# Kernel optimization log

Hardware: AMD Instinct MI355X
Metric: run time of the kernel (lower is better)

The kernel has to match this reference:

```python
import jax, jax.numpy as jnp
import numpy as np

N_HEAD = 8
N_EMBD = 768
T_MAX = 1024


def setup_inputs() -> dict:
    key = jax.random.key(0)
    ks = jax.random.split(key, 5)
    B, T, C = 8, 1024, N_EMBD
    x = jax.random.normal(ks[0], (B, T, C), dtype=jnp.float32)
    c_attn_weight = jax.random.normal(ks[1], (3 * C, C), dtype=jnp.float32) * (1.0 / np.sqrt(C))
    c_attn_bias = jax.random.normal(ks[2], (3 * C,), dtype=jnp.float32) * 0.02
    c_proj_weight = jax.random.normal(ks[3], (C, C), dtype=jnp.float32) * (1.0 / np.sqrt(C))
    c_proj_bias = jax.random.normal(ks[4], (C,), dtype=jnp.float32) * 0.02
    bias = jnp.tril(jnp.ones((T_MAX, T_MAX), dtype=jnp.int32))[None, None]  # (1,1,Tmax,Tmax)
    return {
        "x": x,
        "c_attn_weight": c_attn_weight,
        "c_attn_bias": c_attn_bias,
        "c_proj_weight": c_proj_weight,
        "c_proj_bias": c_proj_bias,
        "bias": bias,
    }


def reference(x, c_attn_weight, c_attn_bias, c_proj_weight, c_proj_bias, bias):
    B, T, C = x.shape
    H = N_HEAD
    D = C // H  # head dim
    qkv = jnp.einsum("btc,fc->btf", x, c_attn_weight) + c_attn_bias  # (B,T,3C)
    q, k, v = jnp.split(qkv, 3, axis=-1)
    q = q.reshape(B, T, H, D).transpose(0, 2, 1, 3)  # (B,H,T,D)
    k = k.reshape(B, T, H, D).transpose(0, 2, 1, 3)
    v = v.reshape(B, T, H, D).transpose(0, 2, 1, 3)
    att = jnp.einsum("bhqd,bhkd->bhqk", q, k) * (1.0 / np.sqrt(D))  # (B,H,T,T)
    mask = bias[:, :, :T, :T] == 0
    att = jnp.where(mask, jnp.float32(-jnp.inf), att)
    att = jax.nn.softmax(att, axis=-1)
    y = jnp.einsum("bhqk,bhkd->bhqd", att, v)  # (B,H,T,D)
    y = y.transpose(0, 2, 1, 3).reshape(B, T, C)
    y = jnp.einsum("btc,fc->btf", y, c_proj_weight) + c_proj_bias
    return y
```

## Files before the change

### kernel.cpp

```cpp
#include <hip/hip_runtime.h>
#include <hip/hip_bf16.h>
#include <stdint.h>


typedef unsigned short ushort_t;
typedef __attribute__((ext_vector_type(8))) short short8;
typedef __attribute__((ext_vector_type(4))) float floatx4;
typedef __attribute__((ext_vector_type(4))) unsigned short ushort4v;

#define MFMA16(a, b, c) __builtin_amdgcn_mfma_f32_16x16x32_bf16(a, b, c, 0, 0, 0)
#define NEG_BIG (-1e30f)

__device__ __forceinline__ unsigned short f2bf(float f) {
  union { float f; unsigned int u; } v; v.f = f;
  unsigned int r = (v.u + 0x7FFFu + ((v.u >> 16) & 1u)) >> 16;
  return (unsigned short)r;
}

__device__ __forceinline__ unsigned int packbf2(float a, float b) {
  union { __hip_bfloat162 h; unsigned int u; } cv;
  cv.h = __float22bfloat162_rn(make_float2(a, b));
  return cv.u;
}

#define GLOAD16(src, dst)                                              \
  __builtin_amdgcn_global_load_lds(                                    \
      (const __attribute__((address_space(1))) void*)(src),            \
      (__attribute__((address_space(3))) void*)(dst), 16, 0, 0)

#define WAITBAR_LGKM(VM)                                               \
  do {                                                                 \
    asm volatile("s_waitcnt vmcnt(" #VM ") lgkmcnt(0)" ::: "memory");  \
    __builtin_amdgcn_s_barrier();                                      \
  } while (0)

__global__ __launch_bounds__(256) void cvt3(
    const float* __restrict__ x, const float* __restrict__ wa,
    const float* __restrict__ wp, ushort_t* __restrict__ xb,
    ushort_t* __restrict__ wab, ushort_t* __restrict__ wpb)
{
  const int n1 = (8192 * 768) / 4, n2 = (2304 * 768) / 4;
  int i = blockIdx.x * 256 + threadIdx.x;
  const float* in; ushort_t* out;
  if (i < n1)            { in = x;  out = xb; }
  else if (i < n1 + n2)  { in = wa; out = wab; i -= n1; }
  else                   { in = wp; out = wpb; i -= (n1 + n2); }
  float4 v = *(const float4*)(in + (size_t)i * 4);
  ushort4v o;
  o.x = f2bf(v.x); o.y = f2bf(v.y); o.z = f2bf(v.z); o.w = f2bf(v.w);
  *(ushort4v*)(out + (size_t)i * 4) = o;
}

#define GSTAGE(LA, LB, OFF)                                            \
  do {                                                                 \
    GLOAD16(gA + (OFF), &LA[wid * 512]);                               \
    GLOAD16(gA + (OFF) + (size_t)64 * 768, &LA[wid * 512 + 64 * 32]);  \
    GLOAD16(gB + (OFF), &LB[wid * 512]);                               \
    GLOAD16(gB + (OFF) + (size_t)64 * 768, &LB[wid * 512 + 64 * 32]);  \
  } while (0)

#define GSTEP(LA, LB, OFF, STG, VM)                                    \
  do {                                                                 \
    asm volatile("s_waitcnt vmcnt(" #VM ")" ::: "memory");             \
    __builtin_amdgcn_s_barrier();                                      \
    short8 af[4], bf[4];                                               \
    _Pragma("unroll")                                                  \
    for (int t_ = 0; t_ < 4; ++t_) {                                   \
      af[t_] = *(const short8*)&LA[(wm + t_ * 16 + l15) * 32 + sw];    \
      bf[t_] = *(const short8*)&LB[(wn + t_ * 16 + l15) * 32 + sw];    \
    }                                                                  \
    asm volatile("s_waitcnt lgkmcnt(0)" ::: "memory");                 \
    __builtin_amdgcn_s_barrier();                                      \
    if (STG) GSTAGE(LA, LB, OFF);                                      \
    __builtin_amdgcn_s_setprio(1);                                     \
    _Pragma("unroll")                                                  \
    for (int tm = 0; tm < 4; ++tm)                                     \
      _Pragma("unroll")                                                \
      for (int tn = 0; tn < 4; ++tn)                                   \
        acc[tm][tn] = MFMA16(af[tm], bf[tn], acc[tm][tn]);             \
    __builtin_amdgcn_s_setprio(0);                                     \
  } while (0)

#define GK2(T)                                                         \
  GSTEP(As0, Bs0, ((T) + 2) * 32, 1, 4);                               \
  GSTEP(As1, Bs1, ((T) + 3) * 32, 1, 4);

#define GEMM_KLOOP                                                     \
  GSTAGE(As0, Bs0, 0); GSTAGE(As1, Bs1, 32);                           \
  GK2(0) GK2(2) GK2(4) GK2(6) GK2(8) GK2(10)                           \
  GK2(12) GK2(14) GK2(16) GK2(18) GK2(20)                              \
  GSTEP(As0, Bs0, 0, 0, 4);                                            \
  GSTEP(As1, Bs1, 0, 0, 0);

#define GEMM_DECLS                                                     \
  __shared__ ushort_t As0[128 * 32], As1[128 * 32];                    \
  __shared__ ushort_t Bs0[128 * 32], Bs1[128 * 32];                    \
  const int tid  = threadIdx.x;                                        \
  const int lane = tid & 63;                                           \
  const int l15  = lane & 15;                                          \
  const int quad = lane >> 4;                                          \
  const int wid  = tid >> 6;                                           \
  const int m0 = blockIdx.x * 128;                                     \
  const int n0 = blockIdx.y * 128;                                     \
  const int wm = (wid >> 1) * 64;                                      \
  const int wn = (wid & 1) * 64;                                       \
  const int srow = tid >> 2;                                           \
  const int scol = (((tid & 3) ^ ((srow ^ (srow >> 2)) & 3))) * 8;     \
  const int sw = (quad ^ ((l15 ^ (l15 >> 2)) & 3)) * 8;                \
  floatx4 acc[4][4] = {};

__global__ __launch_bounds__(256) void gemm_qkv(
    const ushort_t* __restrict__ A,
    const ushort_t* __restrict__ W,
    const float* __restrict__ bias,
    ushort_t* __restrict__ QK,
    ushort_t* __restrict__ VT)
{
  GEMM_DECLS;

  const ushort_t* gA = A + (size_t)(m0 + srow) * 768 + scol;
  const ushort_t* gB = W + (size_t)(n0 + srow) * 768 + scol;

  GEMM_KLOOP;

  const float QSCALE = 0.10206207261596577f * 1.4426950408889634f;

#pragma unroll
  for (int tn = 0; tn < 4; ++tn) {
    const int gc = n0 + wn + tn * 16 + l15;
    const float bv = bias[gc];
    const bool isv = (gc >= 1536);
    const bool isq = (gc < 768);
    const int hh = (gc - 1536) / 96, dd = (gc - 1536) % 96;
#pragma unroll
    for (int tm = 0; tm < 4; ++tm) {
      const int gr = m0 + wm + tm * 16 + quad * 4;
      if (!isv) {
#pragma unroll
        for (int r = 0; r < 4; ++r) {
          float val = acc[tm][tn][r] + bv;
          if (isq) val *= QSCALE;
          QK[(size_t)(gr + r) * 1536 + gc] = f2bf(val);
        }
      } else {
        const int bb = gr >> 10, tt = gr & 1023;
        const int tt2 = (tt & ~0x1C) | (((tt >> 4) & 1) << 2) |
                        (((tt >> 2) & 3) << 3);
        ushort4v o;
        o.x = f2bf(acc[tm][tn][0] + bv);
        o.y = f2bf(acc[tm][tn][1] + bv);
        o.z = f2bf(acc[tm][tn][2] + bv);
        o.w = f2bf(acc[tm][tn][3] + bv);
        *(ushort4v*)(VT + (((size_t)(bb * 8 + hh)) * 96 + dd) * 1024 + tt2) = o;
      }
    }
  }
}

__global__ __launch_bounds__(256) void gemm_proj(
    const ushort_t* __restrict__ A,
    const ushort_t* __restrict__ W,
    const float* __restrict__ bias,
    float* __restrict__ C,
    int M, int N)
{
  GEMM_DECLS;

  const ushort_t* gA = A + (size_t)(m0 + srow) * 768 + scol;
  const ushort_t* gB = W + (size_t)(n0 + srow) * 768 + scol;

  GEMM_KLOOP;

#pragma unroll
  for (int tn = 0; tn < 4; ++tn) {
    const int gc = n0 + wn + tn * 16 + l15;
    const float bv = bias[gc];
#pragma unroll
    for (int tm = 0; tm < 4; ++tm) {
      const int gr = m0 + wm + tm * 16 + quad * 4;
#pragma unroll
      for (int r = 0; r < 4; ++r)
        C[(size_t)(gr + r) * N + gc] = acc[tm][tn][r] + bv;
    }
  }
}

#define ATTN_COMPUTE(KS, VTC, K0)                                      \
  do {                                                                 \
    floatx4 s[4] = {};                                                 \
    __builtin_amdgcn_s_setprio(1);                                     \
    _Pragma("unroll")                                                  \
    for (int t = 0; t < 4; ++t) {                                      \
      _Pragma("unroll")                                                \
      for (int c = 0; c < 3; ++c) {                                    \
        short8 kf = *(const short8*)                                   \
            &KS[(t * 16 + l15) * 96 + c * 32 + quad * 8];              \
        s[t] = MFMA16(kf, qf[c], s[t]);                                \
      }                                                                \
    }                                                                  \
    __builtin_amdgcn_s_setprio(0);                                     \
    float p[4][4];                                                     \
    if ((K0) + 64 <= q0w) {                                            \
      _Pragma("unroll")                                                \
      for (int t = 0; t < 4; ++t)                                      \
        _Pragma("unroll")                                              \
        for (int j = 0; j < 4; ++j) p[t][j] = s[t][j];                 \
    } else {                                                           \
      const int kq = (K0) + quad * 4;                                  \
      _Pragma("unroll")                                                \
      for (int t = 0; t < 4; ++t)                                      \
        _Pragma("unroll")                                              \
        for (int j = 0; j < 4; ++j)                                    \
          p[t][j] = (kq + t * 16 + j <= rq) ? s[t][j] : NEG_BIG;       \
    }                                                                  \
    float m0v = fmaxf(fmaxf(p[0][0], p[0][1]), fmaxf(p[0][2], p[0][3]));\
    float m1v = fmaxf(fmaxf(p[1][0], p[1][1]), fmaxf(p[1][2], p[1][3]));\
    float m2v = fmaxf(fmaxf(p[2][0], p[2][1]), fmaxf(p[2][2], p[2][3]));\
    float m3v = fmaxf(fmaxf(p[3][0], p[3][1]), fmaxf(p[3][2], p[3][3]));\
    float mt = fmaxf(fmaxf(m0v, m1v), fmaxf(m2v, m3v));                \
    mt = fmaxf(mt, __shfl_xor(mt, 16));                                \
    mt = fmaxf(mt, __shfl_xor(mt, 32));                                \
    if (!__all(mt - m_i <= 8.0f)) {                                    \
      const float mn = fmaxf(m_i, mt);                                 \
      const float al = __builtin_amdgcn_exp2f(m_i - mn);               \
      m_i = mn;                                                        \
      l_i *= al;                                                       \
      _Pragma("unroll")                                                \
      for (int j = 0; j < 4; ++j) {                                    \
        const float alr = __shfl(al, quad * 4 + j);                    \
        _Pragma("unroll")                                              \
        for (int f = 0; f < 6; ++f) O[f][j] *= alr;                    \
      }                                                                \
    }                                                                  \
    float rs = 0.f;                                                    \
    _Pragma("unroll")                                                  \
    for (int t = 0; t < 4; ++t)                                        \
      _Pragma("unroll")                                                \
      for (int j = 0; j < 4; ++j) {                                    \
        p[t][j] = __builtin_amdgcn_exp2f(p[t][j] - m_i);               \
        rs += p[t][j];                                                 \
      }                                                                \
    rs += __shfl_xor(rs, 16);                                          \
    rs += __shfl_xor(rs, 32);                                          \
    l_i += rs;                                                         \
    union { short8 s8; unsigned int u[4]; } pf0, pf1;                  \
    pf0.u[0] = packbf2(p[0][0], p[0][1]);                              \
    pf0.u[1] = packbf2(p[0][2], p[0][3]);                              \
    pf0.u[2] = packbf2(p[1][0], p[1][1]);                              \
    pf0.u[3] = packbf2(p[1][2], p[1][3]);                              \
    pf1.u[0] = packbf2(p[2][0], p[2][1]);                              \
    pf1.u[1] = packbf2(p[2][2], p[2][3]);                              \
    pf1.u[2] = packbf2(p[3][0], p[3][1]);                              \
    pf1.u[3] = packbf2(p[3][2], p[3][3]);                              \
    __builtin_amdgcn_s_setprio(1);                                     \
    _Pragma("unroll")                                                  \
    for (int f = 0; f < 6; ++f) {                                      \
      short8 vf0 = *(const short8*)&VTC[(f * 16 + l15) * 72 + quad * 8];\
      O[f] = MFMA16(pf0.s8, vf0, O[f]);                                \
      short8 vf1 = *(const short8*)                                    \
          &VTC[(f * 16 + l15) * 72 + 32 + quad * 8];                   \
      O[f] = MFMA16(pf1.s8, vf1, O[f]);                                \
    }                                                                  \
    __builtin_amdgcn_s_setprio(0);                                     \
  } while (0)

#define AITER(KS, VTC, KSN, VTN, K0)                                   \
  do {                                                                 \
    const int k0_ = (K0);                                              \
    const int nk_ = k0_ + 64;                                          \
    WAITBAR_LGKM(3);                                                   \
    _Pragma("unroll")                                                  \
    for (int i = 0; i < 3; ++i) {                                      \
      const int e = ke0 + i * 512;                                     \
      const int kr = e / 96, kc = e % 96;                              \
      GLOAD16(QK + (rowbase + nk_ + kr) * 1536 + 768 + qoff + kc,      \
              &KSN[wid * 1536 + i * 512]);                             \
    }                                                                  \
    ATTN_COMPUTE(KS, VTC, k0_);                                        \
    _Pragma("unroll")                                                  \
    for (int g = 0; g < 3; ++g)                                        \
      *(short8*)&VTN[(g * 32 + vd) * 72 + vkc] = vreg[g];              \
    if (nk_ + 64 < kend) {                                             \
      _Pragma("unroll")                                                \
      for (int g = 0; g < 3; ++g)                                      \
        vreg[g] = *(const short8*)                                     \
            (vtb + (size_t)(g * 32 + vd) * 1024 + nk_ + 64 + vkc);     \
    }                                                                  \
  } while (0)

#define AITER_LAST(KS, VTC, K0)                                        \
  do {                                                                 \
    WAITBAR_LGKM(0);                                                   \
    ATTN_COMPUTE(KS, VTC, (K0));                                       \
  } while (0)

__global__ __launch_bounds__(256) void attn_fused(
    const ushort_t* __restrict__ QK,
    const ushort_t* __restrict__ VT,
    ushort_t* __restrict__ y)
{
  __shared__ ushort_t Ks0[64 * 96], Ks1[64 * 96];
  __shared__ ushort_t Vt0[96 * 72], Vt1[96 * 72];

  const int tid  = threadIdx.x;
  const int lane = tid & 63;
  const int l15  = lane & 15;
  const int quad = lane >> 4;
  const int wid  = tid >> 6;

  const int lin = blockIdx.x + (blockIdx.y << 4);
  const int swz = ((lin & 7) << 7) + (lin >> 3);
  const int chunk = 15 - (swz & 15);
  const int bh = swz >> 4;
  const int b = bh >> 3;
  const int h = bh & 7;
  const int qoff = h * 96;

  const int q0w = chunk * 64 + wid * 16;
  const int kend = chunk * 64 + 64;
  const int rq = q0w + l15;

  const size_t rowbase = (size_t)b * 1024;
  const ushort_t* vtb = VT + (size_t)bh * 96 * 1024;

  const int ke0 = wid * 1536 + lane * 8;
  const int vd  = (tid >> 3);
  const int vkc = (tid & 7) * 8;

  short8 qf[3];
#pragma unroll
  for (int c = 0; c < 3; ++c)
    qf[c] = *(const short8*)(QK + (rowbase + q0w + l15) * 1536 + qoff +
                             c * 32 + quad * 8);

  float m_i = NEG_BIG;
  float l_i = 0.f;
  floatx4 O[6] = {};

  short8 vreg[3];

#pragma unroll
  for (int g = 0; g < 3; ++g)
    vreg[g] = *(const short8*)(vtb + (size_t)(g * 32 + vd) * 1024 + vkc);
#pragma unroll
  for (int i = 0; i < 3; ++i) {
    const int e = ke0 + i * 512;
    const int kr = e / 96, kc = e % 96;
    GLOAD16(QK + (rowbase + kr) * 1536 + 768 + qoff + kc,
            &Ks0[wid * 1536 + i * 512]);
  }
#pragma unroll
  for (int g = 0; g < 3; ++g)
    *(short8*)&Vt0[(g * 32 + vd) * 72 + vkc] = vreg[g];
#pragma unroll
  for (int g = 0; g < 3; ++g)
    vreg[g] = *(const short8*)(vtb + (size_t)(g * 32 + vd) * 1024 + 64 + vkc);

  int k0 = 0;
  while (k0 + 128 < kend) {
    AITER(Ks0, Vt0, Ks1, Vt1, k0);
    AITER(Ks1, Vt1, Ks0, Vt0, k0 + 64);
    k0 += 128;
  }
  if (k0 + 64 < kend) {
    AITER(Ks0, Vt0, Ks1, Vt1, k0);
    AITER_LAST(Ks1, Vt1, k0 + 64);
  } else {
    AITER_LAST(Ks0, Vt0, k0);
  }

  float inv[4];
#pragma unroll
  for (int j = 0; j < 4; ++j) {
    const float lj = __shfl(l_i, quad * 4 + j);
    inv[j] = 1.0f / fmaxf(lj, 1e-20f);
  }
#pragma unroll
  for (int j = 0; j < 4; ++j) {
    const size_t row = rowbase + q0w + quad * 4 + j;
#pragma unroll
    for (int f = 0; f < 6; ++f)
      y[row * 768 + qoff + f * 16 + l15] = f2bf(O[f][j] * inv[j]);
  }
}

extern "C" void kernel_launch(void* const* d_in, const int* in_sizes, int n_in,
                              void* d_out, int out_size, void* d_ws, size_t ws_size,
                              hipStream_t stream)
{
  const float* x_f  = (const float*)d_in[0];
  const float* wa_f = (const float*)d_in[1];
  const float* ba_f = (const float*)d_in[2];
  const float* wp_f = (const float*)d_in[3];
  const float* bp_f = (const float*)d_in[4];
  float* out = (float*)d_out;

  ushort_t* xb  = (ushort_t*)d_ws;
  ushort_t* wab = xb  + (size_t)8192 * 768;
  ushort_t* wpb = wab + (size_t)2304 * 768;
  ushort_t* QK  = wpb + (size_t)768 * 768;
  ushort_t* VT  = QK  + (size_t)8192 * 1536;
  ushort_t* yw  = VT  + (size_t)8192 * 768;

  cvt3<<<8448, 256, 0, stream>>>(x_f, wa_f, wp_f, xb, wab, wpb);

  gemm_qkv<<<dim3(64, 18), 256, 0, stream>>>(xb, wab, ba_f, QK, VT);
  attn_fused<<<dim3(16, 64), 256, 0, stream>>>(QK, VT, yw);
  gemm_proj<<<dim3(64, 6), 256, 0, stream>>>(yw, wpb, bp_f, out,
                                             8192, 768);
}
```

Measured before the change: 194.4 us.

## Stage GEMM/attention epilogues through LDS for wide stores; shrink proj tile

The QKV GEMM epilogue for the Q/K columns now writes results into a swizzled LDS tile and then stores them to global memory as 16-byte vectors instead of scattered 2-byte stores. The attention kernel's output is staged the same way through LDS before vectorized stores. The projection GEMM uses a 64x128 tile with its own staging and step macros, which doubles the grid to 768 blocks for better occupancy across CUs. The cost is extra barriers and LDS round trips, plus lower per-block reuse in the projection GEMM.

```diff
diff --git a/kernel.cpp b/kernel.cpp
--- a/kernel.cpp
+++ b/kernel.cpp
@@ -92,23 +92,6 @@
   GSTEP(As0, Bs0, 0, 0, 4);                                            \
   GSTEP(As1, Bs1, 0, 0, 0);
 
-#define GEMM_DECLS                                                     \
-  __shared__ ushort_t As0[128 * 32], As1[128 * 32];                    \
-  __shared__ ushort_t Bs0[128 * 32], Bs1[128 * 32];                    \
-  const int tid  = threadIdx.x;                                        \
-  const int lane = tid & 63;                                           \
-  const int l15  = lane & 15;                                          \
-  const int quad = lane >> 4;                                          \
-  const int wid  = tid >> 6;                                           \
-  const int m0 = blockIdx.x * 128;                                     \
-  const int n0 = blockIdx.y * 128;                                     \
-  const int wm = (wid >> 1) * 64;                                      \
-  const int wn = (wid & 1) * 64;                                       \
-  const int srow = tid >> 2;                                           \
-  const int scol = (((tid & 3) ^ ((srow ^ (srow >> 2)) & 3))) * 8;     \
-  const int sw = (quad ^ ((l15 ^ (l15 >> 2)) & 3)) * 8;                \
-  floatx4 acc[4][4] = {};
-
 __global__ __launch_bounds__(256) void gemm_qkv(
     const ushort_t* __restrict__ A,
     const ushort_t* __restrict__ W,
@@ -116,33 +99,72 @@
     ushort_t* __restrict__ QK,
     ushort_t* __restrict__ VT)
 {
-  GEMM_DECLS;
+  __shared__ ushort_t As0[128 * 32], As1[128 * 32];
+  __shared__ ushort_t Bs0[128 * 32], Bs1[128 * 32];
+  const int tid  = threadIdx.x;
+  const int lane = tid & 63;
+  const int l15  = lane & 15;
+  const int quad = lane >> 4;
+  const int wid  = tid >> 6;
+  const int m0 = blockIdx.x * 128;
+  const int n0 = blockIdx.y * 128;
+  const int wm = (wid >> 1) * 64;
+  const int wn = (wid & 1) * 64;
+  const int srow = tid >> 2;
+  const int scol = (((tid & 3) ^ ((srow ^ (srow >> 2)) & 3))) * 8;
+  const int sw = (quad ^ ((l15 ^ (l15 >> 2)) & 3)) * 8;
+  floatx4 acc[4][4] = {};
 
   const ushort_t* gA = A + (size_t)(m0 + srow) * 768 + scol;
   const ushort_t* gB = W + (size_t)(n0 + srow) * 768 + scol;
 
   GEMM_KLOOP;
 
+  asm volatile("s_waitcnt lgkmcnt(0)" ::: "memory");
+  __builtin_amdgcn_s_barrier();
+
   const float QSCALE = 0.10206207261596577f * 1.4426950408889634f;
 
-#pragma unroll
-  for (int tn = 0; tn < 4; ++tn) {
-    const int gc = n0 + wn + tn * 16 + l15;
-    const float bv = bias[gc];
-    const bool isv = (gc >= 1536);
-    const bool isq = (gc < 768);
-    const int hh = (gc - 1536) / 96, dd = (gc - 1536) % 96;
-#pragma unroll
-    for (int tm = 0; tm < 4; ++tm) {
-      const int gr = m0 + wm + tm * 16 + quad * 4;
-      if (!isv) {
+  if (n0 < 1536) {
+    ushort_t* tb = (wid == 0) ? As0 : (wid == 1) ? As1
+                 : (wid == 2) ? Bs0 : Bs1;
+    const float qs = (n0 < 768) ? QSCALE : 1.0f;
+#pragma unroll
+    for (int tn = 0; tn < 4; ++tn) {
+      const float bv = bias[n0 + wn + tn * 16 + l15];
+#pragma unroll
+      for (int tm = 0; tm < 4; ++tm)
 #pragma unroll
         for (int r = 0; r < 4; ++r) {
-          float val = acc[tm][tn][r] + bv;
-          if (isq) val *= QSCALE;
-          QK[(size_t)(gr + r) * 1536 + gc] = f2bf(val);
+          const int row = tm * 16 + quad * 4 + r;
+          const int byte = (row * 128 + (tn * 16 + l15) * 2) ^
+                           ((row & 7) << 4);
+          *(ushort_t*)((char*)tb + byte) = f2bf((acc[tm][tn][r] + bv) * qs);
         }
-      } else {
+    }
+    asm volatile("s_waitcnt lgkmcnt(0)" ::: "memory");
+    const int trow = lane >> 2, ts = lane & 3;
+#pragma unroll
+    for (int p = 0; p < 4; ++p) {
+      const int row = trow + p * 16;
+      const int swz = (row & 7) << 4;
+#pragma unroll
+      for (int k = 0; k < 2; ++k) {
+        const int byte = (row * 128 + ts * 32 + k * 16) ^ swz;
+        short8 v = *(const short8*)((char*)tb + byte);
+        *(short8*)(QK + (size_t)(m0 + wm + row) * 1536 +
+                   n0 + wn + ts * 16 + k * 8) = v;
+      }
+    }
+  } else {
+#pragma unroll
+    for (int tn = 0; tn < 4; ++tn) {
+      const int gc = n0 + wn + tn * 16 + l15;
+      const float bv = bias[gc];
+      const int hh = (gc - 1536) / 96, dd = (gc - 1536) % 96;
+#pragma unroll
+      for (int tm = 0; tm < 4; ++tm) {
+        const int gr = m0 + wm + tm * 16 + quad * 4;
         const int bb = gr >> 10, tt = gr & 1023;
         const int tt2 = (tt & ~0x1C) | (((tt >> 4) & 1) << 2) |
                         (((tt >> 2) & 3) << 3);
@@ -157,6 +179,40 @@
   }
 }
 
+#define PSTAGE(LA, LB, OFF)                                            \
+  do {                                                                 \
+    GLOAD16(gA + (OFF), &LA[wid * 512]);                               \
+    GLOAD16(gB + (OFF), &LB[wid * 512]);                               \
+    GLOAD16(gB + (OFF) + (size_t)64 * 768, &LB[wid * 512 + 64 * 32]);  \
+  } while (0)
+
+#define PSTEP(LA, LB, OFF, STG, VM)                                    \
+  do {                                                                 \
+    asm volatile("s_waitcnt vmcnt(" #VM ")" ::: "memory");             \
+    __builtin_amdgcn_s_barrier();                                      \
+    short8 af[2], bf[4];                                               \
+    _Pragma("unroll")                                                  \
+    for (int t_ = 0; t_ < 2; ++t_)                                     \
+      af[t_] = *(const short8*)&LA[(wm + t_ * 16 + l15) * 32 + sw];    \
+    _Pragma("unroll")                                                  \
+    for (int t_ = 0; t_ < 4; ++t_)                                     \
+      bf[t_] = *(const short8*)&LB[(wn + t_ * 16 + l15) * 32 + sw];    \
+    asm volatile("s_waitcnt lgkmcnt(0)" ::: "memory");                 \
+    __builtin_amdgcn_s_barrier();                                      \
+    if (STG) PSTAGE(LA, LB, OFF);                                      \
+    __builtin_amdgcn_s_setprio(1);                                     \
+    _Pragma("unroll")                                                  \
+    for (int tm = 0; tm < 2; ++tm)                                     \
+      _Pragma("unroll")                                                \
+      for (int tn = 0; tn < 4; ++tn)                                   \
+        acc[tm][tn] = MFMA16(af[tm], bf[tn], acc[tm][tn]);             \
+    __builtin_amdgcn_s_setprio(0);                                     \
+  } while (0)
+
+#define PK2(T)                                                         \
+  PSTEP(As0, Bs0, ((T) + 2) * 32, 1, 3);                               \
+  PSTEP(As1, Bs1, ((T) + 3) * 32, 1, 3);
+
 __global__ __launch_bounds__(256) void gemm_proj(
     const ushort_t* __restrict__ A,
     const ushort_t* __restrict__ W,
@@ -164,19 +220,37 @@
     float* __restrict__ C,
     int M, int N)
 {
-  GEMM_DECLS;
+  __shared__ ushort_t As0[64 * 32], As1[64 * 32];
+  __shared__ ushort_t Bs0[128 * 32], Bs1[128 * 32];
+  const int tid  = threadIdx.x;
+  const int lane = tid & 63;
+  const int l15  = lane & 15;
+  const int quad = lane >> 4;
+  const int wid  = tid >> 6;
+  const int m0 = blockIdx.x * 64;
+  const int n0 = blockIdx.y * 128;
+  const int wm = (wid >> 1) * 32;
+  const int wn = (wid & 1) * 64;
+  const int srow = tid >> 2;
+  const int scol = (((tid & 3) ^ ((srow ^ (srow >> 2)) & 3))) * 8;
+  const int sw = (quad ^ ((l15 ^ (l15 >> 2)) & 3)) * 8;
+  floatx4 acc[2][4] = {};
 
   const ushort_t* gA = A + (size_t)(m0 + srow) * 768 + scol;
   const ushort_t* gB = W + (size_t)(n0 + srow) * 768 + scol;
 
-  GEMM_KLOOP;
+  PSTAGE(As0, Bs0, 0); PSTAGE(As1, Bs1, 32);
+  PK2(0) PK2(2) PK2(4) PK2(6) PK2(8) PK2(10)
+  PK2(12) PK2(14) PK2(16) PK2(18) PK2(20)
+  PSTEP(As0, Bs0, 0, 0, 3);
+  PSTEP(As1, Bs1, 0, 0, 0);
 
 #pragma unroll
   for (int tn = 0; tn < 4; ++tn) {
     const int gc = n0 + wn + tn * 16 + l15;
     const float bv = bias[gc];
 #pragma unroll
-    for (int tm = 0; tm < 4; ++tm) {
+    for (int tm = 0; tm < 2; ++tm) {
       const int gr = m0 + wm + tm * 16 + quad * 4;
 #pragma unroll
       for (int r = 0; r < 4; ++r)
@@ -369,18 +443,29 @@
     AITER_LAST(Ks0, Vt0, k0);
   }
 
+  asm volatile("s_waitcnt vmcnt(0) lgkmcnt(0)" ::: "memory");
+  __builtin_amdgcn_s_barrier();
+
   float inv[4];
 #pragma unroll
   for (int j = 0; j < 4; ++j) {
     const float lj = __shfl(l_i, quad * 4 + j);
     inv[j] = 1.0f / fmaxf(lj, 1e-20f);
   }
-#pragma unroll
-  for (int j = 0; j < 4; ++j) {
-    const size_t row = rowbase + q0w + quad * 4 + j;
+  ushort_t* tb = &Ks0[wid * 1536];
+#pragma unroll
+  for (int j = 0; j < 4; ++j)
 #pragma unroll
     for (int f = 0; f < 6; ++f)
-      y[row * 768 + qoff + f * 16 + l15] = f2bf(O[f][j] * inv[j]);
+      tb[(quad * 4 + j) * 96 + f * 16 + l15] = f2bf(O[f][j] * inv[j]);
+  asm volatile("s_waitcnt lgkmcnt(0)" ::: "memory");
+
+  const int trow = lane >> 2, ts = lane & 3;
+  const size_t grow = rowbase + q0w + trow;
+#pragma unroll
+  for (int k = 0; k < 3; ++k) {
+    short8 v = *(const short8*)&tb[trow * 96 + ts * 24 + k * 8];
+    *(short8*)(y + grow * 768 + qoff + ts * 24 + k * 8) = v;
   }
 }
 
@@ -406,6 +491,6 @@
 
   gemm_qkv<<<dim3(64, 18), 256, 0, stream>>>(xb, wab, ba_f, QK, VT);
   attn_fused<<<dim3(16, 64), 256, 0, stream>>>(QK, VT, yw);
-  gemm_proj<<<dim3(64, 6), 256, 0, stream>>>(yw, wpb, bp_f, out,
-                                             8192, 768);
-}
+  gemm_proj<<<dim3(128, 6), 256, 0, stream>>>(yw, wpb, bp_f, out,
+                                              8192, 768);
+}
```

New measurement: 202.1 us. 4.0% more time.
